# Performance work log

Hardware: AMD Instinct MI355X
Metric: run time of the kernel (lower is better)

The kernel has to match this reference:

```python
import jax, jax.numpy as jnp
import numpy as np

N_NODES = 100000
N_EDGES = 1600000  # directed, src < dst; to_undirected doubles them
N_GRAPHS = 128
D_IN, D_H, D_FC, N_CLS = 128, 64, 32, 10


def setup_inputs() -> dict:
    key = jax.random.key(0)
    ks = jax.random.split(key, 12)
    x = jax.random.normal(ks[0], (N_NODES, D_IN), dtype=jnp.float32)
    # edges with src < dst so concatenating the flipped copy yields the undirected set
    r = jax.random.randint(ks[1], (2, N_EDGES), 0, N_NODES, dtype=jnp.int64)
    src = jnp.minimum(r[0], r[1])
    dst = jnp.maximum(r[0], r[1])
    dst = jnp.where(src == dst, (dst + 1) % N_NODES, dst)  # avoid pre-existing self loops
    edge_index = jnp.stack([src, dst])
    batch = jnp.sort(jax.random.randint(ks[2], (N_NODES,), 0, N_GRAPHS, dtype=jnp.int64))
    sc = lambda f: 1.0 / jnp.sqrt(jnp.float32(f))
    return {
        "x": x,
        "edge_index": edge_index,
        "batch": batch,
        "W_in": jax.random.normal(ks[3], (D_IN, D_H), jnp.float32) * sc(D_IN),
        "b_in": jnp.zeros((D_H,), jnp.float32),
        "W1": jax.random.normal(ks[4], (D_H, D_H), jnp.float32) * sc(D_H),
        "b1": jnp.zeros((D_H,), jnp.float32),
        "W2": jax.random.normal(ks[5], (D_H, D_H), jnp.float32) * sc(D_H),
        "b2": jnp.zeros((D_H,), jnp.float32),
        "Wf1": jax.random.normal(ks[6], (D_H, D_FC), jnp.float32) * sc(D_H),
        "bf1": jnp.zeros((D_FC,), jnp.float32),
        "Wf2": jax.random.normal(ks[7], (D_FC, N_CLS), jnp.float32) * sc(D_FC),
        "bf2": jnp.zeros((N_CLS,), jnp.float32),
    }


def _gcn_conv(x, W, b, src, dst, dinv, n_nodes):
    # GCNConv: x' = D^{-1/2}(A+I)D^{-1/2} (xW) + b, dinv = deg^{-1/2} incl. self loops
    xw = x @ W
    norm = (dinv[src] * dinv[dst])[:, None]              # [E,1]
    agg = jax.ops.segment_sum(xw[src] * norm, dst, num_segments=n_nodes)
    agg = agg + xw * (dinv * dinv)[:, None]              # self-loop term
    return agg + b


def reference(x, edge_index, batch, W_in, b_in, W1, b1, W2, b2, Wf1, bf1, Wf2, bf2):
    n = x.shape[0]
    # to_undirected: append reversed edges (inputs have src<dst, so no dup dirs)
    src = jnp.concatenate([edge_index[0], edge_index[1]])
    dst = jnp.concatenate([edge_index[1], edge_index[0]])
    # degree including self loop
    deg = 1.0 + jax.ops.segment_sum(jnp.ones_like(dst, dtype=x.dtype), dst, num_segments=n)
    dinv = jax.lax.rsqrt(deg)

    h = jax.nn.relu(x @ W_in + b_in)
    h = jax.nn.relu(_gcn_conv(h, W1, b1, src, dst, dinv, n))
    h = jax.nn.relu(_gcn_conv(h, W2, b2, src, dst, dinv, n))

    # global_mean_pool over graph ids
    sums = jax.ops.segment_sum(h, batch, num_segments=N_GRAPHS)
    cnts = jax.ops.segment_sum(jnp.ones((n,), h.dtype), batch, num_segments=N_GRAPHS)
    pooled = sums / jnp.maximum(cnts, 1.0)[:, None]

    g = jax.nn.relu(pooled @ Wf1 + bf1)
    logits = g @ Wf2 + bf2
    return jax.nn.log_softmax(logits, axis=1)
```

## Files before the change

### kernel.cpp

```cpp
#include <hip/hip_runtime.h>
#include <hip/hip_fp16.h>
#include <math.h>

constexpr int DG  = 128;
constexpr int DIN = 128;
constexpr int DH  = 64;
constexpr int DFC = 32;
constexpr int DC  = 10;
constexpr int CAP    = 80;
constexpr int NB     = 2048;
constexpr int ABLK   = 256;
constexpr int SCAP   = 2048;
constexpr int MAXNPB = 52;

typedef _Float16 f16;
typedef f16  f16x8 __attribute__((ext_vector_type(8)));
typedef float f32x4 __attribute__((ext_vector_type(4)));

__device__ __forceinline__ int swz(int row, int byte_in_row) {
    return row * 128 + (byte_in_row ^ ((row & 7) << 4));
}

__global__ __launch_bounds__(256) void k_hist(const int* __restrict__ src,
                                              const int* __restrict__ dst,
                                              int* __restrict__ histT,
                                              int E, int EPB, int NPB) {
    __shared__ int h[NB];
    for (int i = threadIdx.x; i < NB; i += 256) h[i] = 0;
    __syncthreads();
    int e0 = blockIdx.x * EPB, e1 = min(e0 + EPB, E);
    for (int i = e0 + threadIdx.x; i < e1; i += 256) {
        int u = src[i], v = dst[i];
        atomicAdd(&h[v / NPB], 1);
        atomicAdd(&h[u / NPB], 1);
    }
    __syncthreads();
    for (int i = threadIdx.x; i < NB; i += 256)
        histT[(size_t)i * ABLK + blockIdx.x] = h[i];
}

__global__ __launch_bounds__(256) void k_expand(const int* __restrict__ histT,
                                                int* __restrict__ baseT,
                                                int* __restrict__ ecnt,
                                                float* __restrict__ sums,
                                                int* __restrict__ cnts) {
    __shared__ int s[256];
    int b = blockIdx.x, t = threadIdx.x;
    int v = histT[(size_t)b * ABLK + t];
    s[t] = v;
    __syncthreads();
    for (int o = 1; o < 256; o <<= 1) {
        int tv = (t >= o) ? s[t - o] : 0;
        __syncthreads();
        s[t] += tv;
        __syncthreads();
    }
    int incl = s[t];
    baseT[(size_t)b * ABLK + t] = b * SCAP + incl - v;
    if (t == 255) ecnt[b] = min(incl, SCAP);
    int gid = b * 256 + t;
    if (gid < DG * DH) sums[gid] = 0.0f;
    if (gid < DG) cnts[gid] = 0;
}

__global__ __launch_bounds__(256) void k_binplace(const int* __restrict__ src,
                                                  const int* __restrict__ dst,
                                                  const int* __restrict__ baseT,
                                                  int* __restrict__ staging,
                                                  int E, int EPB, int NPB) {
    __shared__ int lcnt[NB];
    __shared__ int lbase[NB];
    int blk = blockIdx.x;
    for (int i = threadIdx.x; i < NB; i += 256) {
        lcnt[i]  = 0;
        lbase[i] = baseT[(size_t)i * ABLK + blk];
    }
    __syncthreads();
    int e0 = blk * EPB, e1 = min(e0 + EPB, E);
    for (int i = e0 + threadIdx.x; i < e1; i += 256) {
        int u = src[i], v = dst[i];
        int bv = v / NPB, bu = u / NPB;
        int rv = atomicAdd(&lcnt[bv], 1);
        int sv = lbase[bv] + rv;
        if (sv < (bv + 1) * SCAP) staging[sv] = ((v - bv * NPB) << 17) | u;
        int ru = atomicAdd(&lcnt[bu], 1);
        int su = lbase[bu] + ru;
        if (su < (bu + 1) * SCAP) staging[su] = ((u - bu * NPB) << 17) | v;
    }
}

__global__ __launch_bounds__(256) void k_rows(const int* __restrict__ staging,
                                              const int* __restrict__ ecnt,
                                              int* __restrict__ adj,
                                              int* __restrict__ cnt,
                                              float* __restrict__ dinv,
                                              int N, int NPB) {
    __shared__ int rows[MAXNPB * CAP];
    __shared__ int cur[MAXNPB];
    int b = blockIdx.x;
    int nbase = b * NPB;
    int nn = min(NPB, N - nbase);
    if (nn <= 0) return;
    for (int i = threadIdx.x; i < nn; i += 256) cur[i] = 0;
    __syncthreads();
    int s0 = b * SCAP, s1 = s0 + ecnt[b];
    for (int i = s0 + threadIdx.x; i < s1; i += 256) {
        int e  = staging[i];
        int vl = e >> 17;
        int u  = e & 0x1FFFF;
        int p  = atomicAdd(&cur[vl], 1);
        if (p < CAP) rows[vl * CAP + p] = u;
    }
    __syncthreads();
    for (int s = threadIdx.x; s < nn * CAP; s += 256) {
        int node = s / CAP, p = s - node * CAP;
        if (p < min(cur[node], CAP))
            adj[(size_t)(nbase + node) * CAP + p] = rows[s];
    }
    for (int i = threadIdx.x; i < nn; i += 256) {
        int c = cur[i];
        cnt[nbase + i]  = c;
        dinv[nbase + i] = rsqrtf(1.0f + (float)c);
    }
}

__global__ __launch_bounds__(256) void k_wprep(const float* __restrict__ Wi,
                                               const float* __restrict__ W1,
                                               const float* __restrict__ W2,
                                               f16* __restrict__ WiT,
                                               f16* __restrict__ W1T,
                                               f16* __restrict__ W2T) {
    int t = blockIdx.x * 256 + threadIdx.x;
    int stride = gridDim.x * 256;
    for (int i = t; i < DH * DIN; i += stride) {
        int c = i >> 7, k = i & 127;
        WiT[i] = (f16)Wi[k * DH + c];
    }
    for (int i = t; i < DH * DH; i += stride) {
        int c = i >> 6, k = i & 63;
        W1T[i] = (f16)W1[k * DH + c];
        W2T[i] = (f16)W2[k * DH + c];
    }
}

__global__ __launch_bounds__(256) void k_lin2(const float* __restrict__ x,
                                              const f16* __restrict__ WiT,
                                              const float* __restrict__ bi,
                                              const f16* __restrict__ W1T,
                                              const float* __restrict__ dinv,
                                              __half* __restrict__ out, int n) {
    __shared__ f16 h0[4 * 16 * 64];
    int t = threadIdx.x, lane = t & 63, w = t >> 6;
    int rb = blockIdx.x * 64 + w * 16;
    if (rb >= n) return;
    int lr = lane & 15;
    int lg = lane >> 4;
    f16x8 a[4];
    const float* xrow = x + (size_t)(rb + lr) * DIN + lg * 8;
#pragma unroll
    for (int k0 = 0; k0 < 4; k0++) {
        float4 f0 = *(const float4*)(xrow + k0 * 32);
        float4 f1 = *(const float4*)(xrow + k0 * 32 + 4);
        a[k0][0] = (f16)f0.x; a[k0][1] = (f16)f0.y; a[k0][2] = (f16)f0.z; a[k0][3] = (f16)f0.w;
        a[k0][4] = (f16)f1.x; a[k0][5] = (f16)f1.y; a[k0][6] = (f16)f1.z; a[k0][7] = (f16)f1.w;
    }
    char* hwb = (char*)(h0 + w * 16 * 64);
#pragma unroll
    for (int cb = 0; cb < 4; cb++) {
        f32x4 acc = {0.f, 0.f, 0.f, 0.f};
        const f16* wt = WiT + (cb * 16 + lr) * DIN + lg * 8;
#pragma unroll
        for (int k0 = 0; k0 < 4; k0++) {
            f16x8 bf = *(const f16x8*)(wt + k0 * 32);
            acc = __builtin_amdgcn_mfma_f32_16x16x32_f16(a[k0], bf, acc, 0, 0, 0);
        }
        float bv = bi[cb * 16 + lr];
#pragma unroll
        for (int r = 0; r < 4; r++) {
            int row = lg * 4 + r;
            *(f16*)(hwb + swz(row, (cb * 16 + lr) * 2)) = (f16)fmaxf(acc[r] + bv, 0.0f);
        }
    }
    f16x8 a2[2];
#pragma unroll
    for (int k0 = 0; k0 < 2; k0++)
        a2[k0] = *(const f16x8*)(hwb + swz(lr, k0 * 64 + lg * 16));
    float dv[4];
#pragma unroll
    for (int r = 0; r < 4; r++) dv[r] = dinv[rb + lg * 4 + r];
#pragma unroll
    for (int cb = 0; cb < 4; cb++) {
        f32x4 acc = {0.f, 0.f, 0.f, 0.f};
        const f16* wt = W1T + (cb * 16 + lr) * DH + lg * 8;
        acc = __builtin_amdgcn_mfma_f32_16x16x32_f16(a2[0], *(const f16x8*)(wt), acc, 0, 0, 0);
        acc = __builtin_amdgcn_mfma_f32_16x16x32_f16(a2[1], *(const f16x8*)(wt + 32), acc, 0, 0, 0);
#pragma unroll
        for (int r = 0; r < 4; r++)
            out[(size_t)(rb + lg * 4 + r) * DH + cb * 16 + lr] = __float2half(acc[r] * dv[r]);
    }
}

__global__ __launch_bounds__(256) void k_mm64(const __half* __restrict__ h,
                                              const f16* __restrict__ WT,
                                              const float* __restrict__ dinv,
                                              __half* __restrict__ out, int n) {
    int t = threadIdx.x, lane = t & 63, w = t >> 6;
    int rb = blockIdx.x * 64 + w * 16;
    if (rb >= n) return;
    int lr = lane & 15, lg = lane >> 4;
    const f16* hp = (const f16*)h + (size_t)(rb + lr) * DH + lg * 8;
    f16x8 a0 = *(const f16x8*)(hp);
    f16x8 a1 = *(const f16x8*)(hp + 32);
    float dv[4];
#pragma unroll
    for (int r = 0; r < 4; r++) dv[r] = dinv[rb + lg * 4 + r];
#pragma unroll
    for (int cb = 0; cb < 4; cb++) {
        const f16* wt = WT + (cb * 16 + lr) * DH + lg * 8;
        f32x4 acc = {0.f, 0.f, 0.f, 0.f};
        acc = __builtin_amdgcn_mfma_f32_16x16x32_f16(a0, *(const f16x8*)(wt), acc, 0, 0, 0);
        acc = __builtin_amdgcn_mfma_f32_16x16x32_f16(a1, *(const f16x8*)(wt + 32), acc, 0, 0, 0);
#pragma unroll
        for (int r = 0; r < 4; r++)
            out[(size_t)(rb + lg * 4 + r) * DH + cb * 16 + lr] = __float2half(acc[r] * dv[r]);
    }
}

__global__ __launch_bounds__(256) void k_gather(const int* __restrict__ cnt,
                                                const int* __restrict__ adj,
                                                const __half2* __restrict__ xws,
                                                const float* __restrict__ dinv,
                                                const float* __restrict__ b,
                                                __half* __restrict__ out, int n) {
    int lane = threadIdx.x & 63;
    int v    = blockIdx.x * 4 + (threadIdx.x >> 6);
    if (v >= n) return;
    int half_id = lane >> 5, fp = lane & 31;
    int len = min(cnt[v], CAP);
    const int* row = adj + (size_t)v * CAP;
    int idx = 0;
    if (lane < len) idx = row[lane];
    int len64 = min(len, 64);
    const char* xb = (const char*)xws;
    int fpo = fp << 2;
    float ax = 0.f, ay = 0.f;
    int k = half_id;
    for (; k + 14 < len64; k += 16) {
        int u0 = __shfl(idx, k);
        int u1 = __shfl(idx, k + 2);
        int u2 = __shfl(idx, k + 4);
        int u3 = __shfl(idx, k + 6);
        int u4 = __shfl(idx, k + 8);
        int u5 = __shfl(idx, k + 10);
        int u6 = __shfl(idx, k + 12);
        int u7 = __shfl(idx, k + 14);
        __half2 h0 = *(const __half2*)(xb + ((u0 << 7) | fpo));
        __half2 h1 = *(const __half2*)(xb + ((u1 << 7) | fpo));
        __half2 h2 = *(const __half2*)(xb + ((u2 << 7) | fpo));
        __half2 h3 = *(const __half2*)(xb + ((u3 << 7) | fpo));
        h0 = __hadd2(h0, *(const __half2*)(xb + ((u4 << 7) | fpo)));
        h1 = __hadd2(h1, *(const __half2*)(xb + ((u5 << 7) | fpo)));
        h2 = __hadd2(h2, *(const __half2*)(xb + ((u6 << 7) | fpo)));
        h3 = __hadd2(h3, *(const __half2*)(xb + ((u7 << 7) | fpo)));
        float2 f0 = __half22float2(h0);
        float2 f1 = __half22float2(h1);
        float2 f2 = __half22float2(h2);
        float2 f3 = __half22float2(h3);
        ax += (f0.x + f1.x) + (f2.x + f3.x);
        ay += (f0.y + f1.y) + (f2.y + f3.y);
    }
    for (; k < len64; k += 2) {
        int u0 = __shfl(idx, k);
        float2 f0 = __half22float2(*(const __half2*)(xb + ((u0 << 7) | fpo)));
        ax += f0.x; ay += f0.y;
    }
    for (int j = 64 + half_id; j < len; j += 2) {
        float2 f0 = __half22float2(xws[(size_t)row[j] * 32 + fp]);
        ax += f0.x; ay += f0.y;
    }
    ax += __shfl_xor(ax, 32);
    ay += __shfl_xor(ay, 32);
    if (half_id == 0) {
        float2 s  = __half22float2(xws[(size_t)v * 32 + fp]);
        float  dv = dinv[v];
        float2 bb = ((const float2*)b)[fp];
        __half2 o = __floats2half2_rn(fmaxf(dv * (ax + s.x) + bb.x, 0.0f),
                                      fmaxf(dv * (ay + s.y) + bb.y, 0.0f));
        ((__half2*)out)[(size_t)v * 32 + fp] = o;
    }
}

__global__ __launch_bounds__(256) void k_pool(const __half* __restrict__ h,
                                              const int* __restrict__ batch,
                                              float* __restrict__ sums,
                                              int* __restrict__ cnts, int n) {
    int lane = threadIdx.x & 63;
    int w    = blockIdx.x * 4 + (threadIdx.x >> 6);
    int start = w * 64;
    if (start >= n) return;
    int end  = min(start + 64, n);
    int curg = batch[start];
    float acc = 0.f;
    int   c   = 0;
    for (int node = start; node < end; node++) {
        int g = batch[node];
        if (g != curg) {
            atomicAdd(&sums[curg * DH + lane], acc);
            if (lane == 0) atomicAdd(&cnts[curg], c);
            acc = 0.f; c = 0; curg = g;
        }
        acc += __half2float(h[(size_t)node * DH + lane]);
        c++;
    }
    atomicAdd(&sums[curg * DH + lane], acc);
    if (lane == 0) atomicAdd(&cnts[curg], c);
}

__global__ __launch_bounds__(64) void k_head(const float* __restrict__ sums,
                                             const int* __restrict__ cnts,
                                             const float* __restrict__ Wf1,
                                             const float* __restrict__ bf1,
                                             const float* __restrict__ Wf2,
                                             const float* __restrict__ bf2,
                                             float* __restrict__ out) {
    int g = blockIdx.x, lane = threadIdx.x;
    float cnt    = (float)max(cnts[g], 1);
    float pooled = sums[g * DH + lane] / cnt;
    float acc = (lane < DFC) ? bf1[lane] : 0.f;
    for (int k = 0; k < DH; k++) {
        float pk = __shfl(pooled, k);
        if (lane < DFC) acc = fmaf(pk, Wf1[k * DFC + lane], acc);
    }
    float gv = fmaxf(acc, 0.f);
    float acc2 = (lane < DC) ? bf2[lane] : 0.f;
    for (int k = 0; k < DFC; k++) {
        float gk = __shfl(gv, k);
        if (lane < DC) acc2 = fmaf(gk, Wf2[k * DC + lane], acc2);
    }
    float v = (lane < DC) ? acc2 : -INFINITY;
    float m = v;
    for (int o = 8; o; o >>= 1) m = fmaxf(m, __shfl_xor(m, o));
    float e = (lane < DC) ? expf(v - m) : 0.f;
    float s = e;
    for (int o = 8; o; o >>= 1) s += __shfl_xor(s, o);
    if (lane < DC) out[g * DC + lane] = v - m - logf(s);
}

extern "C" void kernel_launch(void* const* d_in, const int* in_sizes, int n_in,
                              void* d_out, int out_size, void* d_ws, size_t ws_size,
                              hipStream_t stream) {
    const float* x    = (const float*)d_in[0];
    const int*   ei   = (const int*)d_in[1];
    const int*   batch= (const int*)d_in[2];
    const float* W_in = (const float*)d_in[3];
    const float* b_in = (const float*)d_in[4];
    const float* W1   = (const float*)d_in[5];
    const float* b1   = (const float*)d_in[6];
    const float* W2   = (const float*)d_in[7];
    const float* b2   = (const float*)d_in[8];
    const float* Wf1  = (const float*)d_in[9];
    const float* bf1  = (const float*)d_in[10];
    const float* Wf2  = (const float*)d_in[11];
    const float* bf2  = (const float*)d_in[12];
    float* out = (float*)d_out;

    const int E = in_sizes[1] / 2;
    const int N = in_sizes[0] / DIN;
    const int* src = ei;
    const int* dst = ei + E;

    const int NPB = (N + NB - 1) / NB;
    const int NBU = (N + NPB - 1) / NPB;
    const int EPB = (E + ABLK - 1) / ABLK;

    char* ws = (char*)d_ws;
    size_t off = 0;
    auto alloc = [&](size_t bytes) -> void* {
        void* p = ws + off;
        off = (off + bytes + 255) & ~(size_t)255;
        return p;
    };
    int*    cnt     = (int*)   alloc((size_t)N * 4);
    float*  dinv    = (float*) alloc((size_t)N * 4);
    int*    adj     = (int*)   alloc((size_t)N * CAP * 4);
    int*    histT   = (int*)   alloc((size_t)ABLK * NB * 4);
    int*    baseT   = (int*)   alloc((size_t)ABLK * NB * 4);
    int*    ecnt    = (int*)   alloc((size_t)NB * 4);
    int*    staging = (int*)   alloc((size_t)NB * SCAP * 4);
    __half* hA      = (__half*)alloc((size_t)N * DH * 2);
    __half* hX      = (__half*)alloc((size_t)N * DH * 2);
    float*  sums    = (float*) alloc((size_t)DG * DH * 4);
    int*    cnts    = (int*)   alloc((size_t)DG * 4);
    f16*    WiT     = (f16*)   alloc((size_t)DH * DIN * 2);
    f16*    W1T     = (f16*)   alloc((size_t)DH * DH * 2);
    f16*    W2T     = (f16*)   alloc((size_t)DH * DH * 2);

    k_wprep<<<32, 256, 0, stream>>>(W_in, W1, W2, WiT, W1T, W2T);

    k_hist<<<ABLK, 256, 0, stream>>>(src, dst, histT, E, EPB, NPB);
    k_expand<<<NB, 256, 0, stream>>>(histT, baseT, ecnt, sums, cnts);
    k_binplace<<<ABLK, 256, 0, stream>>>(src, dst, baseT, staging, E, EPB, NPB);
    k_rows<<<NBU, 256, 0, stream>>>(staging, ecnt, adj, cnt, dinv, N, NPB);

    k_lin2<<<(N + 63) / 64, 256, 0, stream>>>(x, WiT, b_in, W1T, dinv, hX, N);

    k_gather<<<(N + 3) / 4, 256, 0, stream>>>(cnt, adj, (const __half2*)hX, dinv, b1, hA, N);

    k_mm64<<<(N + 63) / 64, 256, 0, stream>>>(hA, W2T, dinv, hX, N);
    k_gather<<<(N + 3) / 4, 256, 0, stream>>>(cnt, adj, (const __half2*)hX, dinv, b2, hA, N);

    int pw = (N + 63) / 64;
    k_pool<<<(pw + 3) / 4, 256, 0, stream>>>(hA, batch, sums, cnts, N);

    k_head<<<DG, 64, 0, stream>>>(sums, cnts, Wf1, bf1, Wf2, bf2, out);
}
```

Before: 289.9 us.

## Fuse GCN gathers with second linear and mean pooling, fix node bin size

The first neighbor gather now writes each warp's 16 aggregated rows to swizzled shared memory and multiplies them by W2 with MFMA in the same kernel, which removes the separate k_mm64 pass and its round trip through global memory. The second gather accumulates per-graph sums and counts directly, replacing the separate pooling kernel and the write and reread of the final hidden activations. Node binning switches to a fixed 64 nodes per bin, using shifts and masks instead of integer division, with a larger staging capacity per bin. In exchange, each warp now processes 16 nodes one after another, so there are far fewer warps to hide gather latency, and the unrolled nodes must still respect the bounds when N is not a multiple of 16.

```diff
diff --git a/kernel.cpp b/kernel.cpp
--- a/kernel.cpp
+++ b/kernel.cpp
@@ -7,11 +7,11 @@
 constexpr int DH  = 64;
 constexpr int DFC = 32;
 constexpr int DC  = 10;
-constexpr int CAP    = 80;
-constexpr int NB     = 2048;
-constexpr int ABLK   = 256;
-constexpr int SCAP   = 2048;
-constexpr int MAXNPB = 52;
+constexpr int CAP  = 80;
+constexpr int NPB  = 64;
+constexpr int NB   = 1563;
+constexpr int ABLK = 256;
+constexpr int SCAP = 2560;
 
 typedef _Float16 f16;
 typedef f16  f16x8 __attribute__((ext_vector_type(8)));
@@ -24,15 +24,15 @@
 __global__ __launch_bounds__(256) void k_hist(const int* __restrict__ src,
                                               const int* __restrict__ dst,
                                               int* __restrict__ histT,
-                                              int E, int EPB, int NPB) {
+                                              int E, int EPB) {
     __shared__ int h[NB];
     for (int i = threadIdx.x; i < NB; i += 256) h[i] = 0;
     __syncthreads();
     int e0 = blockIdx.x * EPB, e1 = min(e0 + EPB, E);
     for (int i = e0 + threadIdx.x; i < e1; i += 256) {
         int u = src[i], v = dst[i];
-        atomicAdd(&h[v / NPB], 1);
-        atomicAdd(&h[u / NPB], 1);
+        atomicAdd(&h[v >> 6], 1);
+        atomicAdd(&h[u >> 6], 1);
     }
     __syncthreads();
     for (int i = threadIdx.x; i < NB; i += 256)
@@ -67,7 +67,7 @@
                                                   const int* __restrict__ dst,
                                                   const int* __restrict__ baseT,
                                                   int* __restrict__ staging,
-                                                  int E, int EPB, int NPB) {
+                                                  int E, int EPB) {
     __shared__ int lcnt[NB];
     __shared__ int lbase[NB];
     int blk = blockIdx.x;
@@ -79,13 +79,13 @@
     int e0 = blk * EPB, e1 = min(e0 + EPB, E);
     for (int i = e0 + threadIdx.x; i < e1; i += 256) {
         int u = src[i], v = dst[i];
-        int bv = v / NPB, bu = u / NPB;
+        int bv = v >> 6, bu = u >> 6;
         int rv = atomicAdd(&lcnt[bv], 1);
         int sv = lbase[bv] + rv;
-        if (sv < (bv + 1) * SCAP) staging[sv] = ((v - bv * NPB) << 17) | u;
+        if (sv < (bv + 1) * SCAP) staging[sv] = ((v & 63) << 17) | u;
         int ru = atomicAdd(&lcnt[bu], 1);
         int su = lbase[bu] + ru;
-        if (su < (bu + 1) * SCAP) staging[su] = ((u - bu * NPB) << 17) | v;
+        if (su < (bu + 1) * SCAP) staging[su] = ((u & 63) << 17) | v;
     }
 }
 
@@ -94,9 +94,9 @@
                                               int* __restrict__ adj,
                                               int* __restrict__ cnt,
                                               float* __restrict__ dinv,
-                                              int N, int NPB) {
-    __shared__ int rows[MAXNPB * CAP];
-    __shared__ int cur[MAXNPB];
+                                              int N) {
+    __shared__ int rows[NPB * CAP];
+    __shared__ int cur[NPB];
     int b = blockIdx.x;
     int nbase = b * NPB;
     int nn = min(NPB, N - nbase);
@@ -200,50 +200,17 @@
     }
 }
 
-__global__ __launch_bounds__(256) void k_mm64(const __half* __restrict__ h,
-                                              const f16* __restrict__ WT,
-                                              const float* __restrict__ dinv,
-                                              __half* __restrict__ out, int n) {
-    int t = threadIdx.x, lane = t & 63, w = t >> 6;
-    int rb = blockIdx.x * 64 + w * 16;
-    if (rb >= n) return;
-    int lr = lane & 15, lg = lane >> 4;
-    const f16* hp = (const f16*)h + (size_t)(rb + lr) * DH + lg * 8;
-    f16x8 a0 = *(const f16x8*)(hp);
-    f16x8 a1 = *(const f16x8*)(hp + 32);
-    float dv[4];
-#pragma unroll
-    for (int r = 0; r < 4; r++) dv[r] = dinv[rb + lg * 4 + r];
-#pragma unroll
-    for (int cb = 0; cb < 4; cb++) {
-        const f16* wt = WT + (cb * 16 + lr) * DH + lg * 8;
-        f32x4 acc = {0.f, 0.f, 0.f, 0.f};
-        acc = __builtin_amdgcn_mfma_f32_16x16x32_f16(a0, *(const f16x8*)(wt), acc, 0, 0, 0);
-        acc = __builtin_amdgcn_mfma_f32_16x16x32_f16(a1, *(const f16x8*)(wt + 32), acc, 0, 0, 0);
-#pragma unroll
-        for (int r = 0; r < 4; r++)
-            out[(size_t)(rb + lg * 4 + r) * DH + cb * 16 + lr] = __float2half(acc[r] * dv[r]);
-    }
-}
-
-__global__ __launch_bounds__(256) void k_gather(const int* __restrict__ cnt,
-                                                const int* __restrict__ adj,
-                                                const __half2* __restrict__ xws,
-                                                const float* __restrict__ dinv,
-                                                const float* __restrict__ b,
-                                                __half* __restrict__ out, int n) {
-    int lane = threadIdx.x & 63;
-    int v    = blockIdx.x * 4 + (threadIdx.x >> 6);
-    if (v >= n) return;
-    int half_id = lane >> 5, fp = lane & 31;
+__device__ __forceinline__ void gather_node(int v, const int* __restrict__ cnt,
+                                            const int* __restrict__ adj,
+                                            const char* __restrict__ xb,
+                                            int lane, int half_id, int fpo,
+                                            float& ax, float& ay) {
     int len = min(cnt[v], CAP);
     const int* row = adj + (size_t)v * CAP;
     int idx = 0;
     if (lane < len) idx = row[lane];
     int len64 = min(len, 64);
-    const char* xb = (const char*)xws;
-    int fpo = fp << 2;
-    float ax = 0.f, ay = 0.f;
+    ax = 0.f; ay = 0.f;
     int k = half_id;
     for (; k + 14 < len64; k += 16) {
         int u0 = __shfl(idx, k);
@@ -275,45 +242,101 @@
         ax += f0.x; ay += f0.y;
     }
     for (int j = 64 + half_id; j < len; j += 2) {
-        float2 f0 = __half22float2(xws[(size_t)row[j] * 32 + fp]);
+        float2 f0 = __half22float2(*(const __half2*)(xb + ((row[j] << 7) | fpo)));
         ax += f0.x; ay += f0.y;
     }
     ax += __shfl_xor(ax, 32);
     ay += __shfl_xor(ay, 32);
-    if (half_id == 0) {
-        float2 s  = __half22float2(xws[(size_t)v * 32 + fp]);
+}
+
+__global__ __launch_bounds__(256) void k_g1(const int* __restrict__ cnt,
+                                            const int* __restrict__ adj,
+                                            const __half2* __restrict__ xws,
+                                            const float* __restrict__ dinv,
+                                            const float* __restrict__ b,
+                                            const f16* __restrict__ W2T,
+                                            __half* __restrict__ out, int n) {
+    __shared__ char ht[4 * 2048];
+    int t = threadIdx.x, lane = t & 63, w = t >> 6;
+    int rb = blockIdx.x * 64 + w * 16;
+    if (rb >= n) return;
+    int half_id = lane >> 5, fp = lane & 31, fpo = fp << 2;
+    const char* xb = (const char*)xws;
+    char* wb = ht + w * 2048;
+#pragma unroll 1
+    for (int i = 0; i < 16; i++) {
+        int v = rb + i;
+        float ax, ay;
+        gather_node(v, cnt, adj, xb, lane, half_id, fpo, ax, ay);
+        if (half_id == 0) {
+            float2 s  = __half22float2(*(const __half2*)(xb + ((v << 7) | fpo)));
+            float  dv = dinv[v];
+            float2 bb = ((const float2*)b)[fp];
+            __half2 hh = __floats2half2_rn(fmaxf(dv * (ax + s.x) + bb.x, 0.0f),
+                                           fmaxf(dv * (ay + s.y) + bb.y, 0.0f));
+            *(__half2*)(wb + swz(i, fpo)) = hh;
+        }
+    }
+    int lr = lane & 15, lg = lane >> 4;
+    f16x8 a0 = *(const f16x8*)(wb + swz(lr, lg * 16));
+    f16x8 a1 = *(const f16x8*)(wb + swz(lr, 64 + lg * 16));
+    float dvr[4];
+#pragma unroll
+    for (int r = 0; r < 4; r++) dvr[r] = dinv[rb + lg * 4 + r];
+#pragma unroll
+    for (int cb = 0; cb < 4; cb++) {
+        const f16* wt = W2T + (cb * 16 + lr) * DH + lg * 8;
+        f32x4 acc = {0.f, 0.f, 0.f, 0.f};
+        acc = __builtin_amdgcn_mfma_f32_16x16x32_f16(a0, *(const f16x8*)(wt), acc, 0, 0, 0);
+        acc = __builtin_amdgcn_mfma_f32_16x16x32_f16(a1, *(const f16x8*)(wt + 32), acc, 0, 0, 0);
+#pragma unroll
+        for (int r = 0; r < 4; r++)
+            out[(size_t)(rb + lg * 4 + r) * DH + cb * 16 + lr] = __float2half(acc[r] * dvr[r]);
+    }
+}
+
+__global__ __launch_bounds__(256) void k_g2(const int* __restrict__ cnt,
+                                            const int* __restrict__ adj,
+                                            const __half2* __restrict__ xws,
+                                            const float* __restrict__ dinv,
+                                            const float* __restrict__ b,
+                                            const int* __restrict__ batch,
+                                            float* __restrict__ sums,
+                                            int* __restrict__ cnts, int n) {
+    int t = threadIdx.x, lane = t & 63, w = t >> 6;
+    int rb = blockIdx.x * 64 + w * 16;
+    if (rb >= n) return;
+    int half_id = lane >> 5, fp = lane & 31, fpo = fp << 2;
+    const char* xb = (const char*)xws;
+    int curg = -1, c = 0;
+    float pax = 0.f, pay = 0.f;
+#pragma unroll 1
+    for (int i = 0; i < 16; i++) {
+        int v = rb + i;
+        float ax, ay;
+        gather_node(v, cnt, adj, xb, lane, half_id, fpo, ax, ay);
+        float2 s  = __half22float2(*(const __half2*)(xb + ((v << 7) | fpo)));
         float  dv = dinv[v];
         float2 bb = ((const float2*)b)[fp];
-        __half2 o = __floats2half2_rn(fmaxf(dv * (ax + s.x) + bb.x, 0.0f),
-                                      fmaxf(dv * (ay + s.y) + bb.y, 0.0f));
-        ((__half2*)out)[(size_t)v * 32 + fp] = o;
-    }
-}
-
-__global__ __launch_bounds__(256) void k_pool(const __half* __restrict__ h,
-                                              const int* __restrict__ batch,
-                                              float* __restrict__ sums,
-                                              int* __restrict__ cnts, int n) {
-    int lane = threadIdx.x & 63;
-    int w    = blockIdx.x * 4 + (threadIdx.x >> 6);
-    int start = w * 64;
-    if (start >= n) return;
-    int end  = min(start + 64, n);
-    int curg = batch[start];
-    float acc = 0.f;
-    int   c   = 0;
-    for (int node = start; node < end; node++) {
-        int g = batch[node];
+        float ox = fmaxf(dv * (ax + s.x) + bb.x, 0.0f);
+        float oy = fmaxf(dv * (ay + s.y) + bb.y, 0.0f);
+        int g = batch[v];
         if (g != curg) {
-            atomicAdd(&sums[curg * DH + lane], acc);
-            if (lane == 0) atomicAdd(&cnts[curg], c);
-            acc = 0.f; c = 0; curg = g;
+            if (curg >= 0 && half_id == 0) {
+                atomicAdd(&sums[curg * DH + 2 * fp],     pax);
+                atomicAdd(&sums[curg * DH + 2 * fp + 1], pay);
+                if (lane == 0) atomicAdd(&cnts[curg], c);
+            }
+            curg = g; pax = 0.f; pay = 0.f; c = 0;
         }
-        acc += __half2float(h[(size_t)node * DH + lane]);
+        if (half_id == 0) { pax += ox; pay += oy; }
         c++;
     }
-    atomicAdd(&sums[curg * DH + lane], acc);
-    if (lane == 0) atomicAdd(&cnts[curg], c);
+    if (curg >= 0 && half_id == 0) {
+        atomicAdd(&sums[curg * DH + 2 * fp],     pax);
+        atomicAdd(&sums[curg * DH + 2 * fp + 1], pay);
+        if (lane == 0) atomicAdd(&cnts[curg], c);
+    }
 }
 
 __global__ __launch_bounds__(64) void k_head(const float* __restrict__ sums,
@@ -369,7 +392,6 @@
     const int* src = ei;
     const int* dst = ei + E;
 
-    const int NPB = (N + NB - 1) / NB;
     const int NBU = (N + NPB - 1) / NPB;
     const int EPB = (E + ABLK - 1) / ABLK;
 
@@ -383,8 +405,8 @@
     int*    cnt     = (int*)   alloc((size_t)N * 4);
     float*  dinv    = (float*) alloc((size_t)N * 4);
     int*    adj     = (int*)   alloc((size_t)N * CAP * 4);
-    int*    histT   = (int*)   alloc((size_t)ABLK * NB * 4);
-    int*    baseT   = (int*)   alloc((size_t)ABLK * NB * 4);
+    int*    histT   = (int*)   alloc((size_t)NB * ABLK * 4);
+    int*    baseT   = (int*)   alloc((size_t)NB * ABLK * 4);
     int*    ecnt    = (int*)   alloc((size_t)NB * 4);
     int*    staging = (int*)   alloc((size_t)NB * SCAP * 4);
     __half* hA      = (__half*)alloc((size_t)N * DH * 2);
@@ -397,20 +419,16 @@
 
     k_wprep<<<32, 256, 0, stream>>>(W_in, W1, W2, WiT, W1T, W2T);
 
-    k_hist<<<ABLK, 256, 0, stream>>>(src, dst, histT, E, EPB, NPB);
+    k_hist<<<ABLK, 256, 0, stream>>>(src, dst, histT, E, EPB);
     k_expand<<<NB, 256, 0, stream>>>(histT, baseT, ecnt, sums, cnts);
-    k_binplace<<<ABLK, 256, 0, stream>>>(src, dst, baseT, staging, E, EPB, NPB);
-    k_rows<<<NBU, 256, 0, stream>>>(staging, ecnt, adj, cnt, dinv, N, NPB);
+    k_binplace<<<ABLK, 256, 0, stream>>>(src, dst, baseT, staging, E, EPB);
+    k_rows<<<NBU, 256, 0, stream>>>(staging, ecnt, adj, cnt, dinv, N);
 
     k_lin2<<<(N + 63) / 64, 256, 0, stream>>>(x, WiT, b_in, W1T, dinv, hX, N);
 
-    k_gather<<<(N + 3) / 4, 256, 0, stream>>>(cnt, adj, (const __half2*)hX, dinv, b1, hA, N);
-
-    k_mm64<<<(N + 63) / 64, 256, 0, stream>>>(hA, W2T, dinv, hX, N);
-    k_gather<<<(N + 3) / 4, 256, 0, stream>>>(cnt, adj, (const __half2*)hX, dinv, b2, hA, N);
-
-    int pw = (N + 63) / 64;
-    k_pool<<<(pw + 3) / 4, 256, 0, stream>>>(hA, batch, sums, cnts, N);
+    k_g1<<<(N + 63) / 64, 256, 0, stream>>>(cnt, adj, (const __half2*)hX, dinv, b1, W2T, hA, N);
+
+    k_g2<<<(N + 63) / 64, 256, 0, stream>>>(cnt, adj, (const __half2*)hA, dinv, b2, batch, sums, cnts, N);
 
     k_head<<<DG, 64, 0, stream>>>(sums, cnts, Wf1, bf1, Wf2, bf2, out);
 }
```

Result: faster. 267.0 us (-7.9%).
